# Optimization experiments

Hardware: AMD Instinct MI355X
Metric: run time of the kernel (lower is better)

## Reference

```python
import jax, jax.numpy as jnp
import numpy as np

BATCH = 4096
DIM = 512
TEMP = 0.5

def setup_inputs() -> dict:
    key = jax.random.key(0)
    k1, k2 = jax.random.split(key)
    emb_i = jax.random.normal(k1, (BATCH, DIM), dtype=jnp.float32)
    emb_j = jax.random.normal(k2, (BATCH, DIM), dtype=jnp.float32)
    return {"emb_i": emb_i, "emb_j": emb_j}

def reference(emb_i, emb_j):
    n = emb_i.shape[0]
    # L2-normalize once (torch F.normalize uses eps=1e-12 clamp on norm)
    z_i = emb_i / jnp.maximum(jnp.linalg.norm(emb_i, axis=1, keepdims=True), 1e-12)
    z_j = emb_j / jnp.maximum(jnp.linalg.norm(emb_j, axis=1, keepdims=True), 1e-12)
    z = jnp.concatenate([z_i, z_j], axis=0)            # [2N, D]
    sim = jnp.einsum('nd,md->nm', z, z)                # cosine sim, single GEMM
    # positives: diag(sim, +N) and diag(sim, -N) == rowwise dot(z_i, z_j)
    pos_ij = jnp.sum(z_i * z_j, axis=1)                # [N]
    positives = jnp.concatenate([pos_ij, pos_ij], 0)   # [2N]
    exp_sim = jnp.exp(sim / TEMP)
    mask = 1.0 - jnp.eye(2 * n, dtype=sim.dtype)
    denom = jnp.sum(mask * exp_sim, axis=1)            # [2N]
    loss_partial = -(positives / TEMP - jnp.log(denom))
    return jnp.sum(loss_partial) / (2 * n)
```

## Files before the change

### kernel.cpp

```cpp
#include <hip/hip_runtime.h>
#include <hip/hip_bf16.h>

#define N_ROWS 4096
#define DIM 512
#define TWO_N 8192
#define NTILE 64
#define NTRI  (NTILE * (NTILE + 1) / 2)

typedef float f32x4 __attribute__((ext_vector_type(4)));
typedef long long ll2 __attribute__((ext_vector_type(2)));

__device__ inline void g2l16(const void* g, void* l) {
    __builtin_amdgcn_global_load_lds(
        (const __attribute__((address_space(1))) void*)g,
        (__attribute__((address_space(3))) void*)l,
        16, 0, 0);
}

__global__ void normalize_kernel(const float* __restrict__ ei,
                                 const float* __restrict__ ej,
                                 unsigned char* __restrict__ zq,
                                 float* __restrict__ pos,
                                 float* __restrict__ denom,
                                 float* __restrict__ out) {
    int r = blockIdx.x;
    int t = threadIdx.x;
    const float2 vi = ((const float2*)(ei + (size_t)r * DIM))[t];
    const float2 vj = ((const float2*)(ej + (size_t)r * DIM))[t];
    float si  = vi.x * vi.x + vi.y * vi.y;
    float sj  = vj.x * vj.x + vj.y * vj.y;
    float sij = vi.x * vj.x + vi.y * vj.y;

    for (int o = 32; o; o >>= 1) {
        si  += __shfl_down(si, o);
        sj  += __shfl_down(sj, o);
        sij += __shfl_down(sij, o);
    }
    __shared__ float red[3][4];
    int wave = t >> 6, lane = t & 63;
    if (lane == 0) { red[0][wave] = si; red[1][wave] = sj; red[2][wave] = sij; }
    __syncthreads();
    si  = red[0][0] + red[0][1] + red[0][2] + red[0][3];
    sj  = red[1][0] + red[1][1] + red[1][2] + red[1][3];
    sij = red[2][0] + red[2][1] + red[2][2] + red[2][3];

    float rni = 1.0f / fmaxf(sqrtf(si), 1e-12f);
    float rnj = 1.0f / fmaxf(sqrtf(sj), 1e-12f);
    if (t == 0) {
        pos[r] = sij * rni * rnj;
        denom[r] = 0.0f;
        denom[r + N_ROWS] = 0.0f;
        if (r == 0) out[0] = 0.0f;
    }
    int pi8 = __builtin_amdgcn_cvt_pk_fp8_f32(vi.x * rni, vi.y * rni, 0, false);
    int pj8 = __builtin_amdgcn_cvt_pk_fp8_f32(vj.x * rnj, vj.y * rnj, 0, false);

    int kt   = t >> 6;
    int s8   = (t & 63) >> 2;
    int p    = ((s8 >> 3) << 2) | (s8 & 3);
    int half = (s8 >> 2) & 1;
    int idx16 = kt * 64 + p * 8 + half * 4 + (t & 3);

    ((unsigned short*)(zq + (size_t)r * DIM))[idx16] = (unsigned short)pi8;
    ((unsigned short*)(zq + (size_t)(r + N_ROWS) * DIM))[idx16] = (unsigned short)pj8;
}

__global__ __launch_bounds__(256, 4) void gemm_exp_kernel(
        const unsigned char* __restrict__ zq,
        float* __restrict__ denom) {
    const int w = blockIdx.x;
    const int t = (w & 7) * (NTRI / 8) + (w >> 3);
    int by = (int)(0.5f * (2.0f * NTILE + 1.0f -
              sqrtf((2.0f * NTILE + 1.0f) * (2.0f * NTILE + 1.0f) - 8.0f * t)));
    while ((by + 1) * NTILE - ((by + 1) * by) / 2 <= t) ++by;
    while (by * NTILE - (by * (by - 1)) / 2 > t) --by;
    const int bx = by + (t - (by * NTILE - (by * (by - 1)) / 2));

    const int rb = by * 128, cb = bx * 128;
    const bool diag = (rb == cb);

    const int tid  = threadIdx.x;
    const int wave = tid >> 6;
    const int lane = tid & 63;
    const int quad = lane >> 4;
    const int m    = lane & 15;
    const int wm   = (wave >> 1) * 64;
    const int wn   = (wave & 1) * 64;

    __shared__ __align__(16) unsigned char As[128 * 128];
    __shared__ __align__(16) unsigned char Bs[128 * 128];

    f32x4 acc[4][4];
    #pragma unroll
    for (int i = 0; i < 4; ++i)
        #pragma unroll
        for (int j = 0; j < 4; ++j)
            #pragma unroll
            for (int r = 0; r < 4; ++r) acc[i][j][r] = 0.0f;

    const int srow8 = lane >> 3;
    const int sk    = (((lane & 7) ^ srow8) * 16);

    for (int it = 0; it < 4; ++it) {
        if (it) __syncthreads();
        const int k0 = it * 128;
        #pragma unroll
        for (int cc = 0; cc < 4; ++cc) {
            int c   = 4 * wave + cc;
            int row = c * 8 + srow8;
            g2l16(zq + (size_t)(rb + row) * DIM + k0 + sk, As + c * 1024);
            g2l16(zq + (size_t)(cb + row) * DIM + k0 + sk, Bs + c * 1024);
        }
        __syncthreads();

        #pragma unroll
        for (int c = 0; c < 2; ++c) {
            const int sl = ((((c << 2) | quad) ^ (m & 7)) * 16);
            ll2 af[4], bfr[4];
            #pragma unroll
            for (int i = 0; i < 4; ++i)
                af[i] = *(const ll2*)(As + (wm + i * 16 + m) * 128 + sl);
            #pragma unroll
            for (int j = 0; j < 4; ++j)
                bfr[j] = *(const ll2*)(Bs + (wn + j * 16 + m) * 128 + sl);

            #pragma unroll
            for (int i = 0; i < 4; ++i)
                #pragma unroll
                for (int j = 0; j < 4; ++j) {
                    acc[i][j] = __builtin_amdgcn_mfma_f32_16x16x32_fp8_fp8(
                        af[i][0], bfr[j][0], acc[i][j], 0, 0, 0);
                    acc[i][j] = __builtin_amdgcn_mfma_f32_16x16x32_fp8_fp8(
                        af[i][1], bfr[j][1], acc[i][j], 0, 0, 0);
                }
        }
    }

    __syncthreads();

    float* rs = (float*)As;
    float* cs = rs + 128;
    if (tid < 128) { rs[tid] = 0.0f; cs[tid] = 0.0f; }
    __syncthreads();

    float colsum[4] = {0.0f, 0.0f, 0.0f, 0.0f};
    #pragma unroll
    for (int i = 0; i < 4; ++i) {
        #pragma unroll
        for (int r = 0; r < 4; ++r) {
            int lrow = wm + i * 16 + quad * 4 + r;
            int grow = rb + lrow;
            float s = 0.0f;
            #pragma unroll
            for (int j = 0; j < 4; ++j) {
                int gcol = cb + wn + j * 16 + m;
                float v  = __expf(2.0f * acc[i][j][r]);
                v = (grow == gcol) ? 0.0f : v;
                s += v;
                colsum[j] += v;
            }
            s += __shfl_xor(s, 1);
            s += __shfl_xor(s, 2);
            s += __shfl_xor(s, 4);
            s += __shfl_xor(s, 8);
            if (m == 0) atomicAdd(&rs[lrow], s);
        }
    }
    if (!diag) {
        #pragma unroll
        for (int j = 0; j < 4; ++j) {
            float s = colsum[j];
            s += __shfl_xor(s, 16);
            s += __shfl_xor(s, 32);
            if (quad == 0) atomicAdd(&cs[wn + j * 16 + m], s);
        }
    }
    __syncthreads();
    if (tid < 128) {
        atomicAdd(&denom[rb + tid], rs[tid]);
        if (!diag) atomicAdd(&denom[cb + tid], cs[tid]);
    }
}

__global__ void loss_kernel(const float* __restrict__ pos,
                            const float* __restrict__ denom,
                            float* __restrict__ out) {
    int r = blockIdx.x * 256 + threadIdx.x;
    float s = __logf(denom[r]) - 2.0f * pos[r & (N_ROWS - 1)];
    for (int o = 32; o; o >>= 1) s += __shfl_down(s, o);
    __shared__ float red[4];
    int t = threadIdx.x;
    if ((t & 63) == 0) red[t >> 6] = s;
    __syncthreads();
    if (t == 0)
        atomicAdd(out, (red[0] + red[1] + red[2] + red[3]) / (float)TWO_N);
}

extern "C" void kernel_launch(void* const* d_in, const int* in_sizes, int n_in,
                              void* d_out, int out_size, void* d_ws, size_t ws_size,
                              hipStream_t stream) {
    const float* ei = (const float*)d_in[0];
    const float* ej = (const float*)d_in[1];

    unsigned char* zq = (unsigned char*)d_ws;
    float* pos   = (float*)((char*)d_ws + (size_t)TWO_N * DIM);
    float* denom = pos + N_ROWS;
    float* out   = (float*)d_out;

    normalize_kernel<<<N_ROWS, 256, 0, stream>>>(ei, ej, zq, pos, denom, out);
    gemm_exp_kernel<<<NTRI, 256, 0, stream>>>(zq, denom);
    loss_kernel<<<TWO_N / 256, 256, 0, stream>>>(pos, denom, out);
}
```

Measured before the change: 102.5 us.

## Use 128x256 tiles with 512 threads over the upper-triangular similarity matrix

Makes each GEMM block 128 rows by 256 columns with 8 waves, and maps blocks over a staircase upper triangle where each block keeps only entries with column greater than row, using the exp values for both row and column sums. Diagonal tiles no longer need special handling, and larger tiles cut A-tile reloads and the number of blocks. In exchange, blocks near the diagonal do some wasted work and LDS per block grows to 48KB, which lowers the number of resident blocks.

```diff
diff --git a/kernel.cpp b/kernel.cpp
--- a/kernel.cpp
+++ b/kernel.cpp
@@ -4,8 +4,9 @@
 #define N_ROWS 4096
 #define DIM 512
 #define TWO_N 8192
-#define NTILE 64
-#define NTRI  (NTILE * (NTILE + 1) / 2)
+#define NRB   64
+#define NCB   32
+#define NBLK  1056
 
 typedef float f32x4 __attribute__((ext_vector_type(4)));
 typedef long long ll2 __attribute__((ext_vector_type(2)));
@@ -65,30 +66,28 @@
     ((unsigned short*)(zq + (size_t)(r + N_ROWS) * DIM))[idx16] = (unsigned short)pj8;
 }
 
-__global__ __launch_bounds__(256, 4) void gemm_exp_kernel(
+__global__ __launch_bounds__(512) void gemm_exp_kernel(
         const unsigned char* __restrict__ zq,
         float* __restrict__ denom) {
     const int w = blockIdx.x;
-    const int t = (w & 7) * (NTRI / 8) + (w >> 3);
-    int by = (int)(0.5f * (2.0f * NTILE + 1.0f -
-              sqrtf((2.0f * NTILE + 1.0f) * (2.0f * NTILE + 1.0f) - 8.0f * t)));
-    while ((by + 1) * NTILE - ((by + 1) * by) / 2 <= t) ++by;
-    while (by * NTILE - (by * (by - 1)) / 2 > t) --by;
-    const int bx = by + (t - (by * NTILE - (by * (by - 1)) / 2));
-
-    const int rb = by * 128, cb = bx * 128;
-    const bool diag = (rb == cb);
+    int t = (w & 7) * (NBLK / 8) + (w >> 3);
+    int by = 0;
+    while (t >= NCB - (by >> 1)) { t -= NCB - (by >> 1); ++by; }
+    const int cx = (by >> 1) + t;
+
+    const int rb = by * 128;
+    const int cb = cx * 256;
 
     const int tid  = threadIdx.x;
     const int wave = tid >> 6;
     const int lane = tid & 63;
     const int quad = lane >> 4;
     const int m    = lane & 15;
-    const int wm   = (wave >> 1) * 64;
-    const int wn   = (wave & 1) * 64;
+    const int wm   = (wave >> 2) * 64;
+    const int wn   = (wave & 3) * 64;
 
     __shared__ __align__(16) unsigned char As[128 * 128];
-    __shared__ __align__(16) unsigned char Bs[128 * 128];
+    __shared__ __align__(16) unsigned char Bs[256 * 128];
 
     f32x4 acc[4][4];
     #pragma unroll
@@ -105,10 +104,15 @@
         if (it) __syncthreads();
         const int k0 = it * 128;
         #pragma unroll
+        for (int cc = 0; cc < 2; ++cc) {
+            int c   = 2 * wave + cc;
+            int row = c * 8 + srow8;
+            g2l16(zq + (size_t)(rb + row) * DIM + k0 + sk, As + c * 1024);
+        }
+        #pragma unroll
         for (int cc = 0; cc < 4; ++cc) {
             int c   = 4 * wave + cc;
             int row = c * 8 + srow8;
-            g2l16(zq + (size_t)(rb + row) * DIM + k0 + sk, As + c * 1024);
             g2l16(zq + (size_t)(cb + row) * DIM + k0 + sk, Bs + c * 1024);
         }
         __syncthreads();
@@ -140,7 +144,8 @@
 
     float* rs = (float*)As;
     float* cs = rs + 128;
-    if (tid < 128) { rs[tid] = 0.0f; cs[tid] = 0.0f; }
+    if (tid < 128) rs[tid] = 0.0f;
+    else if (tid < 384) cs[tid - 128] = 0.0f;
     __syncthreads();
 
     float colsum[4] = {0.0f, 0.0f, 0.0f, 0.0f};
@@ -155,7 +160,7 @@
             for (int j = 0; j < 4; ++j) {
                 int gcol = cb + wn + j * 16 + m;
                 float v  = __expf(2.0f * acc[i][j][r]);
-                v = (grow == gcol) ? 0.0f : v;
+                v = (gcol > grow) ? v : 0.0f;
                 s += v;
                 colsum[j] += v;
             }
@@ -166,20 +171,16 @@
             if (m == 0) atomicAdd(&rs[lrow], s);
         }
     }
-    if (!diag) {
-        #pragma unroll
-        for (int j = 0; j < 4; ++j) {
-            float s = colsum[j];
-            s += __shfl_xor(s, 16);
-            s += __shfl_xor(s, 32);
-            if (quad == 0) atomicAdd(&cs[wn + j * 16 + m], s);
-        }
-    }
-    __syncthreads();
-    if (tid < 128) {
-        atomicAdd(&denom[rb + tid], rs[tid]);
-        if (!diag) atomicAdd(&denom[cb + tid], cs[tid]);
-    }
+    #pragma unroll
+    for (int j = 0; j < 4; ++j) {
+        float s = colsum[j];
+        s += __shfl_xor(s, 16);
+        s += __shfl_xor(s, 32);
+        if (quad == 0) atomicAdd(&cs[wn + j * 16 + m], s);
+    }
+    __syncthreads();
+    if (tid < 128)      atomicAdd(&denom[rb + tid], rs[tid]);
+    else if (tid < 384) atomicAdd(&denom[cb + tid - 128], cs[tid - 128]);
 }
 
 __global__ void loss_kernel(const float* __restrict__ pos,
@@ -208,6 +209,6 @@
     float* out   = (float*)d_out;
 
     normalize_kernel<<<N_ROWS, 256, 0, stream>>>(ei, ej, zq, pos, denom, out);
-    gemm_exp_kernel<<<NTRI, 256, 0, stream>>>(zq, denom);
+    gemm_exp_kernel<<<NBLK, 512, 0, stream>>>(zq, denom);
     loss_kernel<<<TWO_N / 256, 256, 0, stream>>>(pos, denom, out);
 }
```

Result: slower. 107.9 us (+5.3%).
